# Kernel tuning notes

Hardware: AMD Instinct MI355X
Metric: run time of the kernel (lower is better)

Reference implementation:

```python
import jax, jax.numpy as jnp
import numpy as np

N_NODES = 25000
N_EDGES = 400000
EMBED_DIM = 128
NUM_HEADS = 8
D_K = EMBED_DIM // NUM_HEADS


def setup_inputs() -> dict:
    key = jax.random.key(0)
    ks = jax.random.split(key, 8)
    sc = 1.0 / np.sqrt(EMBED_DIM)
    return {
        "x": jax.random.normal(ks[0], (N_NODES, EMBED_DIM), jnp.float32),
        "edge_index": jax.random.randint(ks[1], (2, N_EDGES), 0, N_NODES),
        "attn_bias": jax.random.normal(ks[2], (N_EDGES, NUM_HEADS), jnp.float32),
        "Wq": jax.random.normal(ks[3], (EMBED_DIM, EMBED_DIM), jnp.float32) * sc,
        "bq": jnp.zeros((EMBED_DIM,), jnp.float32),
        "Wk": jax.random.normal(ks[4], (EMBED_DIM, EMBED_DIM), jnp.float32) * sc,
        "bk": jnp.zeros((EMBED_DIM,), jnp.float32),
        "Wv": jax.random.normal(ks[5], (EMBED_DIM, EMBED_DIM), jnp.float32) * sc,
        "bv": jnp.zeros((EMBED_DIM,), jnp.float32),
        "Wo": jax.random.normal(ks[6], (EMBED_DIM, EMBED_DIM), jnp.float32) * sc,
        "bo": jnp.zeros((EMBED_DIM,), jnp.float32),
    }


def reference(x, edge_index, attn_bias, Wq, bq, Wk, bk, Wv, bv, Wo, bo):
    N = x.shape[0]
    E = edge_index.shape[1]
    H, dk = NUM_HEADS, D_K
    scale = 1.0 / np.sqrt(dk).astype(np.float32)
    dst = edge_index[0]  # query/aggregation node per edge
    src = edge_index[1]  # key/value node per edge

    # project at node level (as torch: linear(x)[index]), then gather per edge
    q = (x @ Wq.T + bq)[dst].reshape(E, H, dk)
    k = (x @ Wk.T + bk)[src].reshape(E, H, dk)
    v = (x @ Wv.T + bv)[src].reshape(E, H, dk)

    logits = scale * jnp.sum(q * k, axis=2) + attn_bias  # [E, H]

    # segment softmax over edges grouped by destination node
    m = jax.ops.segment_max(logits, dst, num_segments=N)     # [N, H]
    e = jnp.exp(logits - m[dst])                              # [E, H]
    z = jax.ops.segment_sum(e, dst, num_segments=N)           # [N, H]
    scores = e / z[dst]                                       # [E, H]

    agg = jax.ops.segment_sum(scores[..., None] * v, dst, num_segments=N)  # [N, H, dk]
    out = agg.reshape(N, H * dk) @ Wo.T + bo                   # [N, embed_dim]
    return out, logits[..., None]
```

## Files before the change

### kernel.cpp

```cpp
#include <hip/hip_runtime.h>
#include <math.h>

#define N_NODES 25000
#define N_EDGES 400000
#define EMBED   128
#define HEADS   8
#define DK      16
#define MAXDEG  96
#define NX (N_NODES * 128)
#define GBLK 391
#define SCAT_BLK 391

typedef __attribute__((ext_vector_type(8))) short bf16x8;
typedef __attribute__((ext_vector_type(4))) float f32x4;
typedef unsigned int uint;
typedef unsigned short ushort;

__device__ inline uint pack2_bf16(float a, float b) {
    union { float f; uint u; } ua, ub;
    ua.f = a; ub.f = b;
    uint ra = (ua.u + 0x7FFFu + ((ua.u >> 16) & 1u)) >> 16;
    uint rb = (ub.u + 0x7FFFu + ((ub.u >> 16) & 1u)) >> 16;
    return (ra & 0xFFFFu) | (rb << 16);
}
__device__ inline ushort cvt_bf16(float a) {
    union { float f; uint u; } ua; ua.f = a;
    return (ushort)((ua.u + 0x7FFFu + ((ua.u >> 16) & 1u)) >> 16);
}
__device__ inline float bf16_lo(uint u) {
    union { uint u; float f; } x; x.u = u << 16; return x.f;
}
__device__ inline float bf16_hi(uint u) {
    union { uint u; float f; } x; x.u = u & 0xFFFF0000u; return x.f;
}

__global__ __launch_bounds__(256) void prep(
    const float* __restrict__ Wq, const float* __restrict__ Wk,
    const float* __restrict__ Wv, const float* __restrict__ Wo,
    ushort* __restrict__ wb, int* __restrict__ deg)
{
    int i = blockIdx.x * 256 + threadIdx.x;
    if (i < N_NODES) deg[i] = 0;
    if (i < 32768) {
        int j = i * 2;
        const float* src = (j < 16384) ? Wq + j
                         : (j < 32768) ? Wk + (j - 16384)
                         : (j < 49152) ? Wv + (j - 32768)
                         :               Wo + (j - 49152);
        float2 v = *reinterpret_cast<const float2*>(src);
        reinterpret_cast<uint*>(wb)[i] = pack2_bf16(v.x, v.y);
    }
}

__global__ __launch_bounds__(256) void gemm_qkv_scatter(
    const float* __restrict__ x, const ushort* __restrict__ Wall,
    const float* __restrict__ bq, const float* __restrict__ bk,
    const float* __restrict__ bv,
    ushort* __restrict__ Qb, ushort* __restrict__ Kb, ushort* __restrict__ Vb,
    const int* __restrict__ ei, int* __restrict__ deg, int2* __restrict__ csr2)
{
    const int bx = blockIdx.x;
    if (bx >= 3 * GBLK) {
        int t = (bx - 3 * GBLK) * 256 + threadIdx.x;
        int e = t * 4;
        if (e < N_EDGES) {
            int4 d = *reinterpret_cast<const int4*>(ei + e);
            int4 s = *reinterpret_cast<const int4*>(ei + N_EDGES + e);
            int p0 = atomicAdd(&deg[d.x], 1);
            if (p0 < MAXDEG) csr2[d.x * MAXDEG + p0] = make_int2(e, s.x);
            int p1 = atomicAdd(&deg[d.y], 1);
            if (p1 < MAXDEG) csr2[d.y * MAXDEG + p1] = make_int2(e + 1, s.y);
            int p2 = atomicAdd(&deg[d.z], 1);
            if (p2 < MAXDEG) csr2[d.z * MAXDEG + p2] = make_int2(e + 2, s.z);
            int p3 = atomicAdd(&deg[d.w], 1);
            if (p3 < MAXDEG) csr2[d.w * MAXDEG + p3] = make_int2(e + 3, s.w);
        }
        return;
    }

    const int which = bx / GBLK;
    const int mb    = bx - which * GBLK;
    const ushort* W = Wall + which * 16384;
    const float* bias = (which == 0) ? bq : (which == 1) ? bk : bv;
    ushort* C = (which == 0) ? Qb : (which == 1) ? Kb : Vb;

    const int lane = threadIdx.x & 63;
    const int wave = threadIdx.x >> 6;
    const int ml   = lane & 15;
    const int quad = lane >> 4;
    const int m0   = mb * 64 + wave * 16;

    int arow = m0 + ml; if (arow >= N_NODES) arow = N_NODES - 1;
    const float* xp = x + arow * 128 + quad * 8;

    bf16x8 af[4];
#pragma unroll
    for (int ks = 0; ks < 4; ++ks) {
        float4 a0 = *reinterpret_cast<const float4*>(xp + ks * 32);
        float4 a1 = *reinterpret_cast<const float4*>(xp + ks * 32 + 4);
        uint* u = reinterpret_cast<uint*>(&af[ks]);
        u[0] = pack2_bf16(a0.x, a0.y); u[1] = pack2_bf16(a0.z, a0.w);
        u[2] = pack2_bf16(a1.x, a1.y); u[3] = pack2_bf16(a1.z, a1.w);
    }

    f32x4 acc[8];
#pragma unroll
    for (int ct = 0; ct < 8; ++ct) acc[ct] = (f32x4){0.f, 0.f, 0.f, 0.f};

#pragma unroll
    for (int ks = 0; ks < 4; ++ks) {
#pragma unroll
        for (int ct = 0; ct < 8; ++ct) {
            bf16x8 bf = *reinterpret_cast<const bf16x8*>(
                W + (ct * 16 + ml) * 128 + ks * 32 + quad * 8);
            acc[ct] = __builtin_amdgcn_mfma_f32_16x16x32_bf16(af[ks], bf, acc[ct], 0, 0, 0);
        }
    }

#pragma unroll
    for (int ct = 0; ct < 8; ++ct) {
        int col = ct * 16 + ml;
        float b = bias[col];
#pragma unroll
        for (int r = 0; r < 4; ++r) {
            int row = m0 + quad * 4 + r;
            if (row < N_NODES)
                C[row * 128 + col] = cvt_bf16(acc[ct][r] + b);
        }
    }
}

__global__ __launch_bounds__(256) void fused_attn_out(
    const ushort* __restrict__ Q2, const ushort* __restrict__ K2,
    const ushort* __restrict__ V2,
    const float* __restrict__ attn_bias,
    const int* __restrict__ deg, const int2* __restrict__ csr2,
    const ushort* __restrict__ Wo2, const float* __restrict__ bo,
    float* __restrict__ logits, float* __restrict__ out)
{
    __shared__ ushort agg_sh[16 * 136];

    const int tid  = threadIdx.x;
    const int lane = tid & 63;
    const int wid  = tid >> 6;
    const int n0 = blockIdx.x * 4;
    const int n  = n0 + wid;
    int dg = deg[n]; if (dg > MAXDEG) dg = MAXDEG;
    const int start = n * MAXDEG;
    const int h  = lane & 7;
    const int es = lane >> 3;
    const int ml   = lane & 15;
    const int quad = lane >> 4;

    if (tid < 204)
        *reinterpret_cast<uint4*>(reinterpret_cast<char*>(agg_sh) + 1088 + tid * 16) =
            make_uint4(0u, 0u, 0u, 0u);

    const uint4* Qu4 = reinterpret_cast<const uint4*>(Q2);
    const uint4* Ku4 = reinterpret_cast<const uint4*>(K2);
    const uint4* Vu4 = reinterpret_cast<const uint4*>(V2);

    uint4 qa = Qu4[n * 16 + h * 2];
    uint4 qb = Qu4[n * 16 + h * 2 + 1];
    float qf[16];
    {
        uint qq[8] = {qa.x, qa.y, qa.z, qa.w, qb.x, qb.y, qb.z, qb.w};
#pragma unroll
        for (int j = 0; j < 8; ++j) {
            qf[2 * j]     = bf16_lo(qq[j]);
            qf[2 * j + 1] = bf16_hi(qq[j]);
        }
    }

    float acc[16];
#pragma unroll
    for (int j = 0; j < 16; ++j) acc[j] = 0.f;
    float z = 0.f;

    if (dg > 0) {
        int2 ep = csr2[start + (es < dg ? es : dg - 1)];
        for (int base = 0; base < dg; base += 8) {
            int e = ep.x, s = ep.y;
            bool valid = (base + es) < dg;

            uint4 k0 = Ku4[s * 16 + h * 2];
            uint4 k1 = Ku4[s * 16 + h * 2 + 1];
            uint4 v0 = Vu4[s * 16 + h * 2];
            uint4 v1 = Vu4[s * 16 + h * 2 + 1];
            float bias = attn_bias[e * 8 + h];

            int nb = base + 8;
            if (nb < dg) {
                int t2 = nb + es; if (t2 >= dg) t2 = dg - 1;
                ep = csr2[start + t2];
            }

            uint kk[8] = {k0.x, k0.y, k0.z, k0.w, k1.x, k1.y, k1.z, k1.w};
            float d = 0.f;
#pragma unroll
            for (int j = 0; j < 8; ++j)
                d += qf[2 * j] * bf16_lo(kk[j]) + qf[2 * j + 1] * bf16_hi(kk[j]);

            float l = 0.25f * d + bias;
            float p = 0.f;
            if (valid) {
                __builtin_nontemporal_store(l, &logits[e * 8 + h]);
                p = __expf(l);
            }
            z += p;

            uint vv[8] = {v0.x, v0.y, v0.z, v0.w, v1.x, v1.y, v1.z, v1.w};
#pragma unroll
            for (int j = 0; j < 8; ++j) {
                acc[2 * j]     += p * bf16_lo(vv[j]);
                acc[2 * j + 1] += p * bf16_hi(vv[j]);
            }
        }
    }

    {
        int bit = (lane >> 5) & 1;
#pragma unroll
        for (int j = 0; j < 8; ++j) {
            float send = bit ? acc[j] : acc[j + 8];
            float keep = bit ? acc[j + 8] : acc[j];
            acc[j] = keep + __shfl_xor(send, 32, 64);
        }
        bit = (lane >> 4) & 1;
#pragma unroll
        for (int j = 0; j < 4; ++j) {
            float send = bit ? acc[j] : acc[j + 4];
            float keep = bit ? acc[j + 4] : acc[j];
            acc[j] = keep + __shfl_xor(send, 16, 64);
        }
        bit = (lane >> 3) & 1;
#pragma unroll
        for (int j = 0; j < 2; ++j) {
            float send = bit ? acc[j] : acc[j + 2];
            float keep = bit ? acc[j + 2] : acc[j];
            acc[j] = keep + __shfl_xor(send, 8, 64);
        }
    }
    z += __shfl_xor(z, 8, 64);
    z += __shfl_xor(z, 16, 64);
    z += __shfl_xor(z, 32, 64);

    float inv = (z > 0.f) ? 1.f / z : 0.f;
    int d_off = ((lane >> 5) & 1) * 8 + ((lane >> 4) & 1) * 4 + ((lane >> 3) & 1) * 2;
    *reinterpret_cast<uint*>(reinterpret_cast<char*>(agg_sh) + wid * 272 +
                             (h * 16 + d_off) * 2) =
        pack2_bf16(acc[0] * inv, acc[1] * inv);

    __syncthreads();

    if (wid == 0) {
        bf16x8 af[4];
#pragma unroll
        for (int ks = 0; ks < 4; ++ks)
            af[ks] = *reinterpret_cast<const bf16x8*>(
                reinterpret_cast<char*>(agg_sh) + ml * 272 + ks * 64 + quad * 16);

        f32x4 oacc[8];
#pragma unroll
        for (int ct = 0; ct < 8; ++ct) oacc[ct] = (f32x4){0.f, 0.f, 0.f, 0.f};

#pragma unroll
        for (int ks = 0; ks < 4; ++ks) {
#pragma unroll
            for (int ct = 0; ct < 8; ++ct) {
                bf16x8 bf = *reinterpret_cast<const bf16x8*>(
                    Wo2 + (ct * 16 + ml) * 128 + ks * 32 + quad * 8);
                oacc[ct] = __builtin_amdgcn_mfma_f32_16x16x32_bf16(af[ks], bf, oacc[ct], 0, 0, 0);
            }
        }

        if (quad == 0) {
#pragma unroll
            for (int ct = 0; ct < 8; ++ct) {
                int col = ct * 16 + ml;
                float b = bo[col];
#pragma unroll
                for (int r = 0; r < 4; ++r)
                    out[(n0 + r) * 128 + col] = oacc[ct][r] + b;
            }
        }
    }
}

extern "C" void kernel_launch(void* const* d_in, const int* in_sizes, int n_in,
                              void* d_out, int out_size, void* d_ws, size_t ws_size,
                              hipStream_t stream)
{
    const float* x         = (const float*)d_in[0];
    const int*   ei        = (const int*)  d_in[1];
    const float* attn_bias = (const float*)d_in[2];
    const float* Wq = (const float*)d_in[3];
    const float* bq = (const float*)d_in[4];
    const float* Wk = (const float*)d_in[5];
    const float* bk = (const float*)d_in[6];
    const float* Wv = (const float*)d_in[7];
    const float* bv = (const float*)d_in[8];
    const float* Wo = (const float*)d_in[9];
    const float* bo = (const float*)d_in[10];

    float* out    = (float*)d_out;
    float* logits = out + N_NODES * EMBED;

    ushort* wb   = (ushort*)d_ws;
    ushort* Qb   = wb + 4 * 16384;
    ushort* Kb   = Qb + NX;
    ushort* Vb   = Kb + NX;
    int* deg     = (int*)(Vb + NX);
    int2* csr2   = (int2*)(deg + N_NODES);

    prep<<<128, 256, 0, stream>>>(Wq, Wk, Wv, Wo, wb, deg);

    gemm_qkv_scatter<<<3 * GBLK + SCAT_BLK, 256, 0, stream>>>(
        x, wb, bq, bk, bv, Qb, Kb, Vb, ei, deg, csr2);

    fused_attn_out<<<N_NODES / 4, 256, 0, stream>>>(Qb, Kb, Vb, attn_bias,
                                                    deg, csr2, wb + 3 * 16384,
                                                    bo, logits, out);
}
```

Before: 185.8 us.

## Scatter attention bias into CSR order and move scatter blocks first

The edge-scatter phase now also copies each edge's 8-head attention bias into a CSR-ordered buffer next to the edge slot. The attention kernel then reads the bias from that buffer instead of a random gather from attn_bias indexed by edge. Scatter blocks are moved to the front of the grid and use one edge per thread. This adds about 77 MB of extra writes and reads of bias data in exchange for contiguous per-node bias reads, and it requires a larger workspace.

After: 196.5 us. 5.8% more time.

```diff
diff --git a/kernel.cpp b/kernel.cpp
--- a/kernel.cpp
+++ b/kernel.cpp
@@ -9,7 +9,7 @@
 #define MAXDEG  96
 #define NX (N_NODES * 128)
 #define GBLK 391
-#define SCAT_BLK 391
+#define SCAT_BLK 1563
 
 typedef __attribute__((ext_vector_type(8))) short bf16x8;
 typedef __attribute__((ext_vector_type(4))) float f32x4;
@@ -57,29 +57,32 @@
     const float* __restrict__ bq, const float* __restrict__ bk,
     const float* __restrict__ bv,
     ushort* __restrict__ Qb, ushort* __restrict__ Kb, ushort* __restrict__ Vb,
-    const int* __restrict__ ei, int* __restrict__ deg, int2* __restrict__ csr2)
+    const int* __restrict__ ei, const float* __restrict__ attn_bias,
+    int* __restrict__ deg, int2* __restrict__ csr2,
+    float* __restrict__ bias_csr)
 {
     const int bx = blockIdx.x;
-    if (bx >= 3 * GBLK) {
-        int t = (bx - 3 * GBLK) * 256 + threadIdx.x;
-        int e = t * 4;
+    if (bx < SCAT_BLK) {
+        int e = bx * 256 + threadIdx.x;
         if (e < N_EDGES) {
-            int4 d = *reinterpret_cast<const int4*>(ei + e);
-            int4 s = *reinterpret_cast<const int4*>(ei + N_EDGES + e);
-            int p0 = atomicAdd(&deg[d.x], 1);
-            if (p0 < MAXDEG) csr2[d.x * MAXDEG + p0] = make_int2(e, s.x);
-            int p1 = atomicAdd(&deg[d.y], 1);
-            if (p1 < MAXDEG) csr2[d.y * MAXDEG + p1] = make_int2(e + 1, s.y);
-            int p2 = atomicAdd(&deg[d.z], 1);
-            if (p2 < MAXDEG) csr2[d.z * MAXDEG + p2] = make_int2(e + 2, s.z);
-            int p3 = atomicAdd(&deg[d.w], 1);
-            if (p3 < MAXDEG) csr2[d.w * MAXDEG + p3] = make_int2(e + 3, s.w);
+            int dst = ei[e];
+            int src = ei[N_EDGES + e];
+            float4 b0 = *reinterpret_cast<const float4*>(attn_bias + e * 8);
+            float4 b1 = *reinterpret_cast<const float4*>(attn_bias + e * 8 + 4);
+            int pos = atomicAdd(&deg[dst], 1);
+            if (pos < MAXDEG) {
+                int slot = dst * MAXDEG + pos;
+                csr2[slot] = make_int2(e, src);
+                *reinterpret_cast<float4*>(bias_csr + slot * 8)     = b0;
+                *reinterpret_cast<float4*>(bias_csr + slot * 8 + 4) = b1;
+            }
         }
         return;
     }
 
-    const int which = bx / GBLK;
-    const int mb    = bx - which * GBLK;
+    const int gi    = bx - SCAT_BLK;
+    const int which = gi / GBLK;
+    const int mb    = gi - which * GBLK;
     const ushort* W = Wall + which * 16384;
     const float* bias = (which == 0) ? bq : (which == 1) ? bk : bv;
     ushort* C = (which == 0) ? Qb : (which == 1) ? Kb : Vb;
@@ -133,7 +136,7 @@
 __global__ __launch_bounds__(256) void fused_attn_out(
     const ushort* __restrict__ Q2, const ushort* __restrict__ K2,
     const ushort* __restrict__ V2,
-    const float* __restrict__ attn_bias,
+    const float* __restrict__ bias_csr,
     const int* __restrict__ deg, const int2* __restrict__ csr2,
     const ushort* __restrict__ Wo2, const float* __restrict__ bo,
     float* __restrict__ logits, float* __restrict__ out)
@@ -178,21 +181,24 @@
     float z = 0.f;
 
     if (dg > 0) {
-        int2 ep = csr2[start + (es < dg ? es : dg - 1)];
+        int slot = (es < dg ? es : dg - 1);
+        int2 ep = csr2[start + slot];
         for (int base = 0; base < dg; base += 8) {
             int e = ep.x, s = ep.y;
+            int sl = slot;
             bool valid = (base + es) < dg;
 
             uint4 k0 = Ku4[s * 16 + h * 2];
             uint4 k1 = Ku4[s * 16 + h * 2 + 1];
             uint4 v0 = Vu4[s * 16 + h * 2];
             uint4 v1 = Vu4[s * 16 + h * 2 + 1];
-            float bias = attn_bias[e * 8 + h];
+            float bias = bias_csr[(start + sl) * 8 + h];
 
             int nb = base + 8;
             if (nb < dg) {
                 int t2 = nb + es; if (t2 >= dg) t2 = dg - 1;
                 ep = csr2[start + t2];
+                slot = t2;
             }
 
             uint kk[8] = {k0.x, k0.y, k0.z, k0.w, k1.x, k1.y, k1.z, k1.w};
@@ -306,19 +312,20 @@
     float* out    = (float*)d_out;
     float* logits = out + N_NODES * EMBED;
 
-    ushort* wb   = (ushort*)d_ws;
-    ushort* Qb   = wb + 4 * 16384;
-    ushort* Kb   = Qb + NX;
-    ushort* Vb   = Kb + NX;
-    int* deg     = (int*)(Vb + NX);
-    int2* csr2   = (int2*)(deg + N_NODES);
+    ushort* wb     = (ushort*)d_ws;
+    ushort* Qb     = wb + 4 * 16384;
+    ushort* Kb     = Qb + NX;
+    ushort* Vb     = Kb + NX;
+    int* deg       = (int*)(Vb + NX);
+    int2* csr2     = (int2*)(deg + N_NODES);
+    float* biascsr = (float*)(csr2 + N_NODES * MAXDEG);
 
     prep<<<128, 256, 0, stream>>>(Wq, Wk, Wv, Wo, wb, deg);
 
-    gemm_qkv_scatter<<<3 * GBLK + SCAT_BLK, 256, 0, stream>>>(
-        x, wb, bq, bk, bv, Qb, Kb, Vb, ei, deg, csr2);
-
-    fused_attn_out<<<N_NODES / 4, 256, 0, stream>>>(Qb, Kb, Vb, attn_bias,
+    gemm_qkv_scatter<<<SCAT_BLK + 3 * GBLK, 256, 0, stream>>>(
+        x, wb, bq, bk, bv, Qb, Kb, Vb, ei, attn_bias, deg, csr2, biascsr);
+
+    fused_attn_out<<<N_NODES / 4, 256, 0, stream>>>(Qb, Kb, Vb, biascsr,
                                                     deg, csr2, wb + 3 * 16384,
                                                     bo, logits, out);
 }
```

## Interleave scatter blocks with GEMM blocks and split output projection across waves

Applied to the files above, without the earlier changes.

The combined QKV GEMM and CSR-scatter kernel now interleaves its blocks: every fourth block does the edge scatter and the other three do GEMM tiles. This mixes memory-atomic work with MFMA work on the GPU at the same time instead of running the scatter blocks at the tail. In the fused attention kernel, the final Wo projection is split across all four waves, each computing two column tiles, instead of leaving waves 1-3 idle while wave 0 does all eight. The risk is that the interleaved block mapping changes access locality for the GEMM tiles.

New measurement: 186.5 us. No clear change (+0.4%).

```diff
diff --git a/kernel.cpp b/kernel.cpp
--- a/kernel.cpp
+++ b/kernel.cpp
@@ -10,6 +10,7 @@
 #define NX (N_NODES * 128)
 #define GBLK 391
 #define SCAT_BLK 391
+#define TOT_BLK (3 * GBLK + SCAT_BLK)
 
 typedef __attribute__((ext_vector_type(8))) short bf16x8;
 typedef __attribute__((ext_vector_type(4))) float f32x4;
@@ -60,8 +61,8 @@
     const int* __restrict__ ei, int* __restrict__ deg, int2* __restrict__ csr2)
 {
     const int bx = blockIdx.x;
-    if (bx >= 3 * GBLK) {
-        int t = (bx - 3 * GBLK) * 256 + threadIdx.x;
+    if ((bx & 3) == 3) {
+        int t = (bx >> 2) * 256 + threadIdx.x;
         int e = t * 4;
         if (e < N_EDGES) {
             int4 d = *reinterpret_cast<const int4*>(ei + e);
@@ -78,8 +79,9 @@
         return;
     }
 
-    const int which = bx / GBLK;
-    const int mb    = bx - which * GBLK;
+    const int gi    = (bx >> 2) * 3 + (bx & 3);
+    const int which = gi / GBLK;
+    const int mb    = gi - which * GBLK;
     const ushort* W = Wall + which * 16384;
     const float* bias = (which == 0) ? bq : (which == 1) ? bk : bv;
     ushort* C = (which == 0) ? Qb : (which == 1) ? Kb : Vb;
@@ -253,35 +255,35 @@
 
     __syncthreads();
 
-    if (wid == 0) {
+    {
         bf16x8 af[4];
 #pragma unroll
         for (int ks = 0; ks < 4; ++ks)
             af[ks] = *reinterpret_cast<const bf16x8*>(
                 reinterpret_cast<char*>(agg_sh) + ml * 272 + ks * 64 + quad * 16);
 
-        f32x4 oacc[8];
-#pragma unroll
-        for (int ct = 0; ct < 8; ++ct) oacc[ct] = (f32x4){0.f, 0.f, 0.f, 0.f};
+        f32x4 oacc[2];
+        oacc[0] = (f32x4){0.f, 0.f, 0.f, 0.f};
+        oacc[1] = (f32x4){0.f, 0.f, 0.f, 0.f};
 
 #pragma unroll
         for (int ks = 0; ks < 4; ++ks) {
 #pragma unroll
-            for (int ct = 0; ct < 8; ++ct) {
+            for (int c = 0; c < 2; ++c) {
                 bf16x8 bf = *reinterpret_cast<const bf16x8*>(
-                    Wo2 + (ct * 16 + ml) * 128 + ks * 32 + quad * 8);
-                oacc[ct] = __builtin_amdgcn_mfma_f32_16x16x32_bf16(af[ks], bf, oacc[ct], 0, 0, 0);
+                    Wo2 + ((wid * 2 + c) * 16 + ml) * 128 + ks * 32 + quad * 8);
+                oacc[c] = __builtin_amdgcn_mfma_f32_16x16x32_bf16(af[ks], bf, oacc[c], 0, 0, 0);
             }
         }
 
         if (quad == 0) {
 #pragma unroll
-            for (int ct = 0; ct < 8; ++ct) {
-                int col = ct * 16 + ml;
+            for (int c = 0; c < 2; ++c) {
+                int col = (wid * 2 + c) * 16 + ml;
                 float b = bo[col];
 #pragma unroll
                 for (int r = 0; r < 4; ++r)
-                    out[(n0 + r) * 128 + col] = oacc[ct][r] + b;
+                    out[(n0 + r) * 128 + col] = oacc[c][r] + b;
             }
         }
     }
@@ -315,7 +317,7 @@
 
     prep<<<128, 256, 0, stream>>>(Wq, Wk, Wv, Wo, wb, deg);
 
-    gemm_qkv_scatter<<<3 * GBLK + SCAT_BLK, 256, 0, stream>>>(
+    gemm_qkv_scatter<<<TOT_BLK, 256, 0, stream>>>(
         x, wb, bq, bk, bv, Qb, Kb, Vb, ei, deg, csr2);
 
     fused_attn_out<<<N_NODES / 4, 256, 0, stream>>>(Qb, Kb, Vb, attn_bias,
```
